# Kernel tuning notes

Hardware: AMD Instinct MI355X
Metric: run time of the kernel (lower is better)

The kernel has to match this reference:

```python
import jax, jax.numpy as jnp
import numpy as np

B, T, HID, H, Dk, Dv, K = 2, 1024, 1024, 8, 128, 128, 4
EPS = 1e-5


def _dwconv_causal(y, w, b):
    # y: [B,T,C], w: [C,1,K], b: [C]; torch Conv1d(padding=K-1) then [:, :, :T] == causal left-pad
    C = y.shape[-1]
    z = jnp.transpose(y, (0, 2, 1))  # [B,C,T]
    z = jax.lax.conv_general_dilated(
        z, w, window_strides=(1,), padding=[(K - 1, 0)],
        feature_group_count=C, dimension_numbers=("NCH", "OIH", "NCH"))
    z = z + b[None, :, None]
    return jnp.transpose(z, (0, 2, 1))


def _forward(x, Wq, Wk, Wv, conv_q_w, conv_q_b, conv_k_w, conv_k_b,
             conv_v_w, conv_v_b, Wa, ba, Wb, bb, Wg, Wo, ln_g, ln_b):
    b_, t_ = x.shape[0], x.shape[1]
    q = jax.nn.silu(_dwconv_causal(x @ Wq, conv_q_w, conv_q_b))
    k = jax.nn.silu(_dwconv_causal(x @ Wk, conv_k_w, conv_k_b))
    v = jax.nn.silu(_dwconv_causal(x @ Wv, conv_v_w, conv_v_b))
    q = q.reshape(b_, t_, H, Dk)
    k = k.reshape(b_, t_, H, Dk) * (Dk ** -0.5)
    v = v.reshape(b_, t_, H, Dv)
    alpha = jax.nn.sigmoid(x @ Wa + ba)  # [B,T,H]
    beta = jax.nn.sigmoid(x @ Wb + bb)   # [B,T,H]

    # time-major for scan
    qt = jnp.transpose(q, (1, 0, 2, 3))  # [T,B,H,Dk]
    kt = jnp.transpose(k, (1, 0, 2, 3))
    vt = jnp.transpose(v, (1, 0, 2, 3))  # [T,B,H,Dv]
    at = jnp.transpose(alpha, (1, 0, 2))  # [T,B,H]
    bt = jnp.transpose(beta, (1, 0, 2))

    def step(S, inp):
        q_t, k_t, v_t, a_t, b_t = inp
        sk = jnp.einsum('bhij,bhj->bhi', S, k_t)          # S @ k
        err = sk - v_t                                     # [B,H,Dv]
        S = a_t[:, :, None, None] * S - b_t[:, :, None, None] * (err[..., None] * k_t[:, :, None, :])
        o_t = jnp.einsum('bhij,bhj->bhi', S, q_t)          # S @ q (post-update)
        return S, o_t

    S0 = jnp.zeros((b_, H, Dv, Dk), x.dtype)
    _, o = jax.lax.scan(step, S0, (qt, kt, vt, at, bt))
    o = jnp.transpose(o, (1, 0, 2, 3))  # [B,T,H,Dv]

    # LayerNorm over Dv
    mu = jnp.mean(o, axis=-1, keepdims=True)
    var = jnp.mean((o - mu) ** 2, axis=-1, keepdims=True)
    o = (o - mu) * jax.lax.rsqrt(var + EPS) * ln_g + ln_b

    g = jax.nn.sigmoid(x @ Wg).reshape(b_, t_, H, Dv)
    o = (o * g).reshape(b_, t_, H * Dv)
    return o @ Wo


def setup_inputs() -> dict:
    key = jax.random.key(0)
    ks = jax.random.split(key, 18)
    s = 0.02

    def n(k, shape, scale=s):
        return jax.random.normal(k, shape, jnp.float32) * scale

    return {
        "x": jax.random.normal(ks[0], (B, T, HID), jnp.float32),
        "Wq": n(ks[1], (HID, H * Dk)),
        "Wk": n(ks[2], (HID, H * Dk)),
        "Wv": n(ks[3], (HID, H * Dv)),
        "conv_q_w": n(ks[4], (H * Dk, 1, K), 0.25),
        "conv_q_b": n(ks[5], (H * Dk,), 0.1),
        "conv_k_w": n(ks[6], (H * Dk, 1, K), 0.25),
        "conv_k_b": n(ks[7], (H * Dk,), 0.1),
        "conv_v_w": n(ks[8], (H * Dv, 1, K), 0.25),
        "conv_v_b": n(ks[9], (H * Dv,), 0.1),
        "Wa": n(ks[10], (HID, H)),
        "ba": n(ks[11], (H,), 0.1),
        "Wb": n(ks[12], (HID, H)),
        "bb": n(ks[13], (H,), 0.1),
        "Wg": n(ks[14], (HID, H * Dv)),
        "Wo": n(ks[15], (H * Dv, HID)),
        "ln_g": jnp.ones((Dv,), jnp.float32),
        "ln_b": jnp.zeros((Dv,), jnp.float32),
    }


def reference(x, Wq, Wk, Wv, conv_q_w, conv_q_b, conv_k_w, conv_k_b,
              conv_v_w, conv_v_b, Wa, ba, Wb, bb, Wg, Wo, ln_g, ln_b):
    return _forward(x, Wq, Wk, Wv, conv_q_w, conv_q_b, conv_k_w, conv_k_b,
                    conv_v_w, conv_v_b, Wa, ba, Wb, bb, Wg, Wo, ln_g, ln_b)
```

## Files before the change

### kernel.cpp

```cpp
#include <hip/hip_runtime.h>

#define TSEQ 1024
#define HID_ 1024
#define NH 8
#define DK 128
#define DV 128
#define ROWS 2048
#define SZf (ROWS * HID_)
#define LCH 64
#define NCK 16
#define KSTR 136
#define ESTR 65

typedef __attribute__((ext_vector_type(8))) short short8;
typedef __attribute__((ext_vector_type(4))) float f32x4;
#define MFMA __builtin_amdgcn_mfma_f32_16x16x32_bf16

__device__ __forceinline__ float sig_(float x) { return 1.f / (1.f + __expf(-x)); }

__device__ __forceinline__ ushort f2bf(float f) {
    unsigned int u = __builtin_bit_cast(unsigned int, f);
    u += 0x7FFF + ((u >> 16) & 1);
    return (ushort)(u >> 16);
}
__device__ __forceinline__ float bf2f(ushort u) {
    return __builtin_bit_cast(float, ((unsigned int)u) << 16);
}
__device__ __forceinline__ unsigned int pk2(float lo, float hi) {
    return (unsigned int)f2bf(lo) | ((unsigned int)f2bf(hi) << 16);
}

__device__ __forceinline__ void gload16(const void* g, void* l) {
    __builtin_amdgcn_global_load_lds(
        (const __attribute__((address_space(1))) unsigned int*)g,
        (__attribute__((address_space(3))) unsigned int*)l, 16, 0, 0);
}

__global__ __launch_bounds__(256)
void k_x2bf(const float* __restrict__ x, ushort* __restrict__ xb)
{
    const size_t i8 = (size_t)blockIdx.x * 256 + threadIdx.x;
    float4 v0 = *(const float4*)(x + i8 * 8);
    float4 v1 = *(const float4*)(x + i8 * 8 + 4);
    uint4 o;
    o.x = pk2(v0.x, v0.y); o.y = pk2(v0.z, v0.w);
    o.z = pk2(v1.x, v1.y); o.w = pk2(v1.z, v1.w);
    *(uint4*)(xb + i8 * 8) = o;
}

__global__ __launch_bounds__(256)
void k_wT(const float* __restrict__ s0, const float* __restrict__ s1,
          const float* __restrict__ s2, const float* __restrict__ s3,
          const float* __restrict__ s4,
          ushort* __restrict__ dst, ushort* __restrict__ dstWo)
{
    const int z = blockIdx.z;
    const float* W = (z == 0) ? s0 : (z == 1) ? s1 : (z == 2) ? s2
                   : (z == 3) ? s3 : s4;
    ushort* WT = (z < 4) ? dst + (size_t)z * (1024 * 1024) : dstWo;
    __shared__ float t[64][65];
    const int n0 = blockIdx.x * 64, k0 = blockIdx.y * 64;
    const int rr = threadIdx.x >> 4, cc = threadIdx.x & 15;
#pragma unroll
    for (int i = 0; i < 4; ++i) {
        const int row = i * 16 + rr;
        float4 v = *(const float4*)(W + (size_t)(k0 + row) * 1024 + n0 + cc * 4);
        t[row][cc * 4 + 0] = v.x; t[row][cc * 4 + 1] = v.y;
        t[row][cc * 4 + 2] = v.z; t[row][cc * 4 + 3] = v.w;
    }
    __syncthreads();
#pragma unroll
    for (int i = 0; i < 4; ++i) {
        const int n = i * 16 + rr;
        const int kc = cc * 4;
        ushort4 o;
        o.x = f2bf(t[kc + 0][n]); o.y = f2bf(t[kc + 1][n]);
        o.z = f2bf(t[kc + 2][n]); o.w = f2bf(t[kc + 3][n]);
        *(ushort4*)(WT + (size_t)(n0 + n) * 1024 + k0 + kc) = o;
    }
}

template<typename CT>
__device__ __forceinline__ void gemm_tile_mfma(const ushort* __restrict__ A,
                                               const ushort* __restrict__ BT,
                                               CT* __restrict__ C,
                                               int brow, int bcol)
{
    __shared__ ushort As[128 * 64];
    __shared__ ushort Bs[128 * 64];
    const int tid  = threadIdx.x;
    const int lane = tid & 63;
    const int wv   = tid >> 6;
    const int wm   = (wv >> 1) * 64;
    const int wn   = (wv & 1) * 64;
    const int l15  = lane & 15;
    const int lq   = lane >> 4;

    f32x4 acc[4][4];
#pragma unroll
    for (int i = 0; i < 4; ++i)
#pragma unroll
        for (int j = 0; j < 4; ++j)
#pragma unroll
            for (int e = 0; e < 4; ++e) acc[i][j][e] = 0.f;

    for (int k0 = 0; k0 < 1024; k0 += 64) {
        __syncthreads();
#pragma unroll
        for (int j = 0; j < 4; ++j) {
            const int idx  = j * 256 + tid;
            const int row  = idx >> 3;
            const int gcol = ((idx & 7) ^ (row & 7)) * 8;
            const int ldst = (j * 256 + wv * 64) * 8;
            gload16(A  + (size_t)(brow + row) * 1024 + k0 + gcol, As + ldst);
            gload16(BT + (size_t)(bcol + row) * 1024 + k0 + gcol, Bs + ldst);
        }
        __syncthreads();
#pragma unroll
        for (int kk = 0; kk < 2; ++kk) {
            short8 af[4], bf[4];
#pragma unroll
            for (int i = 0; i < 4; ++i) {
                const int ra = wm + i * 16 + l15;
                af[i] = *(const short8*)(As + ra * 64 + (((kk * 4 + lq) ^ (ra & 7)) * 8));
            }
#pragma unroll
            for (int j = 0; j < 4; ++j) {
                const int rb = wn + j * 16 + l15;
                bf[j] = *(const short8*)(Bs + rb * 64 + (((kk * 4 + lq) ^ (rb & 7)) * 8));
            }
#pragma unroll
            for (int i = 0; i < 4; ++i)
#pragma unroll
                for (int j = 0; j < 4; ++j)
                    acc[i][j] = MFMA(af[i], bf[j], acc[i][j], 0, 0, 0);
        }
    }
    const int l4 = lane >> 4;
#pragma unroll
    for (int i = 0; i < 4; ++i)
#pragma unroll
        for (int j = 0; j < 4; ++j)
#pragma unroll
            for (int r = 0; r < 4; ++r) {
                const size_t o = (size_t)(brow + wm + i * 16 + l4 * 4 + r) * 1024 +
                                 bcol + wn + j * 16 + l15;
                if constexpr (sizeof(CT) == 2) C[o] = f2bf(acc[i][j][r]);
                else                           C[o] = acc[i][j][r];
            }
}

__global__ __launch_bounds__(256)
void k_gemm4(const ushort* __restrict__ A, const ushort* __restrict__ WT,
             ushort* __restrict__ Cbase)
{
    const ushort* BT = WT + (size_t)blockIdx.z * (1024 * 1024);
    ushort* C = Cbase + (size_t)blockIdx.z * SZf;
    gemm_tile_mfma<ushort>(A, BT, C, blockIdx.y * 128, blockIdx.x * 128);
}

__global__ __launch_bounds__(256)
void k_gemm1(const ushort* __restrict__ A, const ushort* __restrict__ BT,
             float* __restrict__ C)
{
    gemm_tile_mfma<float>(A, BT, C, blockIdx.y * 128, blockIdx.x * 128);
}

__global__ __launch_bounds__(256)
void k_ab(const float* __restrict__ x, const float* __restrict__ Wa,
          const float* __restrict__ ba, const float* __restrict__ Wb,
          const float* __restrict__ bb, float* __restrict__ aT,
          float* __restrict__ bT)
{
    const int r = blockIdx.x * 4 + (threadIdx.x >> 6);
    const int lane = threadIdx.x & 63;
    const int b = r >> 10, t = r & 1023;
    const float* xr = x + (size_t)r * HID_;
    float acc[16];
#pragma unroll
    for (int n = 0; n < 16; ++n) acc[n] = 0.f;
    for (int c = lane; c < HID_; c += 64) {
        const float xv = xr[c];
        const float* wa = Wa + c * 8;
        const float* wb = Wb + c * 8;
#pragma unroll
        for (int n = 0; n < 8; ++n) {
            acc[n]     = fmaf(xv, wa[n], acc[n]);
            acc[8 + n] = fmaf(xv, wb[n], acc[8 + n]);
        }
    }
#pragma unroll
    for (int n = 0; n < 16; ++n) {
#pragma unroll
        for (int m = 32; m; m >>= 1) acc[n] += __shfl_xor(acc[n], m);
    }
    if (lane < 8) {
        aT[(size_t)(b * 8 + lane) * TSEQ + t] = sig_(acc[lane] + ba[lane]);
        bT[(size_t)(b * 8 + lane) * TSEQ + t] = sig_(acc[8 + lane] + bb[lane]);
    }
}

__global__ __launch_bounds__(256)
void k_convprep(const ushort* __restrict__ qb_, const ushort* __restrict__ kb_,
                const ushort* __restrict__ vb_,
                const float* __restrict__ wq, const float* __restrict__ bq,
                const float* __restrict__ wk, const float* __restrict__ bk,
                const float* __restrict__ wv, const float* __restrict__ bv,
                const float* __restrict__ aT, const float* __restrict__ bT,
                ushort* __restrict__ Kst, ushort* __restrict__ Qst,
                ushort* __restrict__ VstT, ushort* __restrict__ KTst,
                ushort* __restrict__ Mg, ushort* __restrict__ Gg,
                float* __restrict__ pug, float* __restrict__ pog,
                float* __restrict__ dtotg)
{
    const int cid = blockIdx.x;
    const int bh = cid >> 4, j = cid & 15;
    const int b = bh >> 3, h = bh & 7;
    const int tid = threadIdx.x;
    const int t0 = j * LCH;

    __shared__ ushort Kb[64 * KSTR], Qb[64 * KSTR];
    __shared__ ushort Vl[128 * 72];
    __shared__ float Ef[64 * ESTR];
    __shared__ float Mf[64 * ESTR];
    __shared__ float cums[64], bv2[64];

    if (tid >= 192) {
        const int lane = tid - 192;
        const float a = aT[(size_t)bh * TSEQ + t0 + lane];
        bv2[lane] = bT[(size_t)bh * TSEQ + t0 + lane];
        float cs = __logf(a);
#pragma unroll
        for (int d = 1; d < 64; d <<= 1) {
            float pv = __shfl_up(cs, d);
            if (lane >= d) cs += pv;
        }
        cums[lane] = cs;
    } else {
        const int z = tid >> 6;
        const int c2 = (tid & 63) * 2;
        const ushort* src  = (z == 0) ? qb_ : (z == 1) ? kb_ : vb_;
        const float* w     = (z == 0) ? wq : (z == 1) ? wk : wv;
        const float* bias  = (z == 0) ? bq : (z == 1) ? bk : bv;
        const float scale  = (z == 1) ? 0.08838834764831845f : 1.f;
        const int gc = h * 128 + c2;
        const float w0a = w[gc * 4],     w1a = w[gc * 4 + 1], w2a = w[gc * 4 + 2], w3a = w[gc * 4 + 3];
        const float w0b = w[gc * 4 + 4], w1b = w[gc * 4 + 5], w2b = w[gc * 4 + 6], w3b = w[gc * 4 + 7];
        const float bsa = bias[gc], bsb = bias[gc + 1];
        float ya0 = 0.f, ya1 = 0.f, ya2 = 0.f, yb0 = 0.f, yb1 = 0.f, yb2 = 0.f;
        if (j > 0) {
#pragma unroll
            for (int i = 0; i < 3; ++i) {
                uint u = *(const uint*)(src + (size_t)(b * TSEQ + t0 - 3 + i) * HID_ + gc);
                const float lo = bf2f((ushort)u), hi = bf2f((ushort)(u >> 16));
                if (i == 0) { ya0 = lo; yb0 = hi; }
                else if (i == 1) { ya1 = lo; yb1 = hi; }
                else { ya2 = lo; yb2 = hi; }
            }
        }
#pragma unroll 4
        for (int tl = 0; tl < 64; ++tl) {
            uint u = *(const uint*)(src + (size_t)(b * TSEQ + t0 + tl) * HID_ + gc);
            const float x0 = bf2f((ushort)u), x1 = bf2f((ushort)(u >> 16));
            float a0 = fmaf(w0a, ya0, fmaf(w1a, ya1, fmaf(w2a, ya2, fmaf(w3a, x0, bsa))));
            float a1 = fmaf(w0b, yb0, fmaf(w1b, yb1, fmaf(w2b, yb2, fmaf(w3b, x1, bsb))));
            const float s0 = a0 * sig_(a0) * scale;
            const float s1 = a1 * sig_(a1) * scale;
            if (z == 0)      *(uint*)(Qb + tl * KSTR + c2) = pk2(s0, s1);
            else if (z == 1) *(uint*)(Kb + tl * KSTR + c2) = pk2(s0, s1);
            else {
                Vl[(c2 + 0) * 72 + tl] = f2bf(s0);
                Vl[(c2 + 1) * 72 + tl] = f2bf(s1);
            }
            ya0 = ya1; ya1 = ya2; ya2 = x0;
            yb0 = yb1; yb1 = yb2; yb2 = x1;
        }
    }
    __syncthreads();

    const size_t go = (size_t)cid * 8192;
    const float ctop = cums[63];
#pragma unroll
    for (int jx = 0; jx < 4; ++jx) {
        const int i16 = tid + jx * 256;
        const int row = i16 >> 4, col = (i16 & 15) * 8;
        *(uint4*)(Kst + go + i16 * 8) = *(const uint4*)(Kb + row * KSTR + col);
        *(uint4*)(Qst + go + i16 * 8) = *(const uint4*)(Qb + row * KSTR + col);
    }
#pragma unroll
    for (int jx = 0; jx < 4; ++jx) {
        const int idx = tid + jx * 256;
        const int dv = idx >> 3, tq = (idx & 7) * 8;
        *(uint4*)(VstT + go + dv * 64 + tq) = *(const uint4*)(Vl + dv * 72 + tq);
        const int dk = idx >> 3, tt = (idx & 7) * 8;
        ushort tmp[8];
#pragma unroll
        for (int e = 0; e < 8; ++e)
            tmp[e] = f2bf(bf2f(Kb[(tt + e) * KSTR + dk]) * __expf(ctop - cums[tt + e]));
        *(uint4*)(KTst + go + dk * 64 + tt) = *(uint4*)tmp;
    }

    const int wv2 = tid >> 6, l = tid & 63, l15 = l & 15, lq = l >> 4;
    const int k8o = lq * 8;
    f32x4 accK[4], accQ4[4];
#pragma unroll
    for (int jx = 0; jx < 4; ++jx) {
        accK[jx] = f32x4{0.f, 0.f, 0.f, 0.f};
        accQ4[jx] = f32x4{0.f, 0.f, 0.f, 0.f};
    }
#pragma unroll
    for (int kk = 0; kk < 4; ++kk) {
        short8 aK = *(const short8*)(Kb + (wv2 * 16 + l15) * KSTR + kk * 32 + k8o);
        short8 aQ = *(const short8*)(Qb + (wv2 * 16 + l15) * KSTR + kk * 32 + k8o);
#pragma unroll
        for (int js = 0; js < 4; ++js) {
            short8 bK = *(const short8*)(Kb + (js * 16 + l15) * KSTR + kk * 32 + k8o);
            accK[js]  = MFMA(aK, bK, accK[js], 0, 0, 0);
            accQ4[js] = MFMA(aQ, bK, accQ4[js], 0, 0, 0);
        }
    }
    ushort* Gc = Gg + (size_t)cid * 4096;
#pragma unroll
    for (int js = 0; js < 4; ++js) {
#pragma unroll
        for (int r = 0; r < 4; ++r) {
            const int t = wv2 * 16 + lq * 4 + r;
            const int s = js * 16 + l15;
            const float cp = (t > 0) ? cums[t - 1] : 0.f;
            Ef[t * ESTR + s] = (s < t) ? __expf(cp - cums[s]) * accK[js][r] : 0.f;
            const float gv = (s <= t) ? __expf(cums[t] - cums[s]) * accQ4[js][r] : 0.f;
            Gc[t * 64 + s] = f2bf(gv);
        }
    }
    __syncthreads();

    if (tid < 64) {
        const int s = tid;
        for (int r = 0; r < 64; ++r) Mf[r * ESTR + s] = 0.f;
        Mf[s * ESTR + s] = bv2[s];
        for (int t = 1; t < 64; ++t) {
            float s0 = 0.f, s1 = 0.f;
            int r = 0;
            for (; r + 1 < t; r += 2) {
                s0 = fmaf(Ef[t * ESTR + r],     Mf[r * ESTR + s],       s0);
                s1 = fmaf(Ef[t * ESTR + r + 1], Mf[(r + 1) * ESTR + s], s1);
            }
            if (r < t) s0 = fmaf(Ef[t * ESTR + r], Mf[r * ESTR + s], s0);
            if (s < t) Mf[t * ESTR + s] = -bv2[t] * (s0 + s1);
        }
    }
    __syncthreads();
    ushort* Mc = Mg + (size_t)cid * 4096;
#pragma unroll
    for (int jx = 0; jx < 16; ++jx) {
        const int e = tid + jx * 256;
        Mc[e] = f2bf(Mf[(e >> 6) * ESTR + (e & 63)]);
    }
    if (tid < 64) {
        const float cp = (tid > 0) ? cums[tid - 1] : 0.f;
        pug[cid * 64 + tid] = __expf(cp);
        pog[cid * 64 + tid] = __expf(cums[tid]);
        if (tid == 0) dtotg[cid] = __expf(cums[63]);
    }
}

__global__ __launch_bounds__(256)
void k_scan2(const ushort* __restrict__ Kst, const ushort* __restrict__ KTst,
             const ushort* __restrict__ VstT, const ushort* __restrict__ Mg,
             const float* __restrict__ pug, const float* __restrict__ dtg,
             ushort* __restrict__ Sst, ushort* __restrict__ Wst)
{
    const int blk = blockIdx.x;
    const int bh = blk >> 1, half = blk & 1;
    const int tid = threadIdx.x;
    const int wv = tid >> 6, l = tid & 63, l15 = l & 15, lq = l >> 4;
    const int k8o = lq * 8;
    const int dvw = wv * 16;

    __shared__ ushort Kb[64 * KSTR];
    __shared__ ushort KTb[128 * 72];
    __shared__ ushort Mb[64 * 72];
    __shared__ ushort Vb[64 * 72];
    __shared__ ushort Shb[64 * KSTR], Slb[64 * KSTR];
    __shared__ ushort Yb[64 * 72], Wb[64 * 72];
    __shared__ float puv[64], dts[1];

    f32x4 accS[8];
#pragma unroll
    for (int m = 0; m < 8; ++m) accS[m] = f32x4{0.f, 0.f, 0.f, 0.f};

    uint4 rk[4], rkt[4], rm[2], rv[2];
    float rpu = 0.f, rdt = 0.f;

    auto LOADC = [&](int cc) {
        const int cid = bh * 16 + cc;
        const size_t go = (size_t)cid * 8192;
#pragma unroll
        for (int jx = 0; jx < 4; ++jx) {
            rk[jx]  = *(const uint4*)(Kst  + go + (tid + jx * 256) * 8);
            rkt[jx] = *(const uint4*)(KTst + go + (tid + jx * 256) * 8);
        }
#pragma unroll
        for (int jx = 0; jx < 2; ++jx) {
            rm[jx] = *(const uint4*)(Mg + (size_t)cid * 4096 + (tid + jx * 256) * 8);
            rv[jx] = *(const uint4*)(VstT + go + half * 4096 + (tid + jx * 256) * 8);
        }
        if (tid < 64) {
            rpu = pug[cid * 64 + tid];
            if (tid == 0) rdt = dtg[cid];
        }
    };
    auto WRITEC = [&]() {
#pragma unroll
        for (int jx = 0; jx < 4; ++jx) {
            const int i16 = tid + jx * 256;
            *(uint4*)(Kb  + (i16 >> 4) * KSTR + (i16 & 15) * 8) = rk[jx];
            *(uint4*)(KTb + (i16 >> 3) * 72   + (i16 & 7) * 8)  = rkt[jx];
        }
#pragma unroll
        for (int jx = 0; jx < 2; ++jx) {
            const int i8 = tid + jx * 256;
            *(uint4*)(Mb + (i8 >> 3) * 72 + (i8 & 7) * 8) = rm[jx];
            *(uint4*)(Vb + (i8 >> 3) * 72 + (i8 & 7) * 8) = rv[jx];
        }
        if (tid < 64) {
            puv[tid] = rpu;
            if (tid == 0) dts[0] = rdt;
        }
    };

    LOADC(0); WRITEC();
    __syncthreads();

    for (int c = 0; c < NCK; ++c) {
        if (c + 1 < NCK) LOADC(c + 1);

#pragma unroll
        for (int m = 0; m < 8; ++m) {
            ushort h4[4], l4v[4];
#pragma unroll
            for (int r = 0; r < 4; ++r) {
                const float sv = accS[m][r];
                const ushort hi = f2bf(sv);
                h4[r] = hi;
                l4v[r] = f2bf(sv - bf2f(hi));
            }
            *(uint2*)(Shb + (dvw + l15) * KSTR + m * 16 + lq * 4) = *(uint2*)h4;
            *(uint2*)(Slb + (dvw + l15) * KSTR + m * 16 + lq * 4) = *(uint2*)l4v;
        }
        f32x4 accU[4];
#pragma unroll
        for (int jj = 0; jj < 4; ++jj) accU[jj] = f32x4{0.f, 0.f, 0.f, 0.f};
#pragma unroll
        for (int kk = 0; kk < 4; ++kk) {
            short8 sh = *(const short8*)(Shb + (dvw + l15) * KSTR + kk * 32 + k8o);
            short8 sl = *(const short8*)(Slb + (dvw + l15) * KSTR + kk * 32 + k8o);
#pragma unroll
            for (int jj = 0; jj < 4; ++jj) {
                short8 ka = *(const short8*)(Kb + (jj * 16 + l15) * KSTR + kk * 32 + k8o);
                accU[jj] = MFMA(ka, sh, accU[jj], 0, 0, 0);
                accU[jj] = MFMA(ka, sl, accU[jj], 0, 0, 0);
            }
        }
#pragma unroll
        for (int jj = 0; jj < 4; ++jj) {
            float pu4[4];
            *(float4*)pu4 = *(const float4*)(puv + jj * 16 + lq * 4);
            ushort v4[4];
            *(uint2*)v4 = *(const uint2*)(Vb + (dvw + l15) * 72 + jj * 16 + lq * 4);
            ushort y4[4];
#pragma unroll
            for (int r = 0; r < 4; ++r)
                y4[r] = f2bf(bf2f(v4[r]) - pu4[r] * accU[jj][r]);
            *(uint2*)(Yb + (dvw + l15) * 72 + jj * 16 + lq * 4) = *(uint2*)y4;
        }
        f32x4 accW[4];
#pragma unroll
        for (int jj = 0; jj < 4; ++jj) accW[jj] = f32x4{0.f, 0.f, 0.f, 0.f};
#pragma unroll
        for (int kk = 0; kk < 2; ++kk) {
            short8 yb = *(const short8*)(Yb + (dvw + l15) * 72 + kk * 32 + k8o);
#pragma unroll
            for (int jj = 0; jj < 4; ++jj) {
                short8 mf = *(const short8*)(Mb + (jj * 16 + l15) * 72 + kk * 32 + k8o);
                accW[jj] = MFMA(mf, yb, accW[jj], 0, 0, 0);
            }
        }
#pragma unroll
        for (int jj = 0; jj < 4; ++jj) {
            ushort w4[4];
#pragma unroll
            for (int r = 0; r < 4; ++r)
                w4[r] = f2bf(accW[jj][r]);
            *(uint2*)(Wb + (dvw + l15) * 72 + jj * 16 + lq * 4) = *(uint2*)w4;
        }
        const float dt = dts[0];
#pragma unroll
        for (int m = 0; m < 8; ++m)
#pragma unroll
            for (int r = 0; r < 4; ++r) accS[m][r] *= dt;
#pragma unroll
        for (int kk = 0; kk < 2; ++kk) {
            short8 wc = *(const short8*)(Wb + (dvw + l15) * 72 + kk * 32 + k8o);
#pragma unroll
            for (int m = 0; m < 8; ++m) {
                short8 kt = *(const short8*)(KTb + (m * 16 + l15) * 72 + kk * 32 + k8o);
                accS[m] = MFMA(kt, wc, accS[m], 0, 0, 0);
            }
        }
        {
            const int cid = bh * 16 + c;
#pragma unroll
            for (int jx = 0; jx < 4; ++jx) {
                const int idx = l + jx * 64;
                const int dvo = idx >> 4, ko = (idx & 15) * 8;
                *(uint4*)(Sst + (size_t)cid * 16384 +
                          (half * 64 + dvw + dvo) * 128 + ko) =
                    *(const uint4*)(Shb + (dvw + dvo) * KSTR + ko);
            }
#pragma unroll
            for (int jx = 0; jx < 2; ++jx) {
                const int idx = l + jx * 64;
                const int dvo = idx >> 3, t8 = (idx & 7) * 8;
                *(uint4*)(Wst + (size_t)cid * 8192 +
                          (half * 64 + dvw + dvo) * 64 + t8) =
                    *(const uint4*)(Wb + (dvw + dvo) * 72 + t8);
            }
        }
        __syncthreads();
        if (c + 1 < NCK) WRITEC();
        __syncthreads();
    }
}

__global__ __launch_bounds__(256)
void k_out(const ushort* __restrict__ Sst, const ushort* __restrict__ Qst,
           const ushort* __restrict__ Gg, const ushort* __restrict__ Wst,
           const float* __restrict__ pog, const ushort* __restrict__ gb_,
           const float* __restrict__ lng, const float* __restrict__ lnb,
           ushort* __restrict__ ogb)
{
    const int cid = blockIdx.x;
    const int bh = cid >> 4, c = cid & 15;
    const int b = bh >> 3, h = bh & 7;
    const int t0 = c * LCH;
    const int tid = threadIdx.x;
    const int wv = tid >> 6, l = tid & 63, l15 = l & 15, lq = l >> 4;
    const int k8o = lq * 8;

    __shared__ ushort Sb[128 * KSTR];
    __shared__ ushort Qb[64 * KSTR];
    __shared__ ushort Gb[64 * 72];
    __shared__ ushort Wqb[128 * 72];
    __shared__ float  Ot[64 * 132];
    __shared__ float  pov[64];

#pragma unroll
    for (int jx = 0; jx < 8; ++jx) {
        const int i16 = tid + jx * 256;
        *(uint4*)(Sb + (i16 >> 4) * KSTR + (i16 & 15) * 8) =
            *(const uint4*)(Sst + (size_t)cid * 16384 + i16 * 8);
    }
#pragma unroll
    for (int jx = 0; jx < 4; ++jx) {
        const int i16 = tid + jx * 256;
        *(uint4*)(Qb + (i16 >> 4) * KSTR + (i16 & 15) * 8) =
            *(const uint4*)(Qst + (size_t)cid * 8192 + i16 * 8);
        *(uint4*)(Wqb + (i16 >> 3) * 72 + (i16 & 7) * 8) =
            *(const uint4*)(Wst + (size_t)cid * 8192 + i16 * 8);
    }
#pragma unroll
    for (int jx = 0; jx < 2; ++jx) {
        const int i8 = tid + jx * 256;
        *(uint4*)(Gb + (i8 >> 3) * 72 + (i8 & 7) * 8) =
            *(const uint4*)(Gg + (size_t)cid * 4096 + i8 * 8);
    }
    if (tid < 64) pov[tid] = pog[cid * 64 + tid];
    __syncthreads();

#pragma unroll
    for (int i = 0; i < 2; ++i) {
        const int dvt = wv * 2 + i;
        f32x4 acc[4], acg[4];
#pragma unroll
        for (int jj = 0; jj < 4; ++jj) {
            acc[jj] = f32x4{0.f, 0.f, 0.f, 0.f};
            acg[jj] = f32x4{0.f, 0.f, 0.f, 0.f};
        }
#pragma unroll
        for (int kk = 0; kk < 4; ++kk) {
            short8 sa = *(const short8*)(Sb + (dvt * 16 + l15) * KSTR + kk * 32 + k8o);
#pragma unroll
            for (int jj = 0; jj < 4; ++jj) {
                short8 qb = *(const short8*)(Qb + (jj * 16 + l15) * KSTR + kk * 32 + k8o);
                acc[jj] = MFMA(sa, qb, acc[jj], 0, 0, 0);
            }
        }
#pragma unroll
        for (int kk = 0; kk < 2; ++kk) {
            short8 wa = *(const short8*)(Wqb + (dvt * 16 + l15) * 72 + kk * 32 + k8o);
#pragma unroll
            for (int jj = 0; jj < 4; ++jj) {
                short8 gb = *(const short8*)(Gb + (jj * 16 + l15) * 72 + kk * 32 + k8o);
                acg[jj] = MFMA(wa, gb, acg[jj], 0, 0, 0);
            }
        }
#pragma unroll
        for (int jj = 0; jj < 4; ++jj) {
            const int t = jj * 16 + l15;
            const float po = pov[t];
            float4 o4;
            o4.x = po * acc[jj][0] + acg[jj][0];
            o4.y = po * acc[jj][1] + acg[jj][1];
            o4.z = po * acc[jj][2] + acg[jj][2];
            o4.w = po * acc[jj][3] + acg[jj][3];
            *(float4*)(Ot + t * 132 + dvt * 16 + lq * 4) = o4;
        }
    }
    __syncthreads();

    const int d = l * 2;
    const float lg0 = lng[d], lg1 = lng[d + 1];
    const float lb0 = lnb[d], lb1 = lnb[d + 1];
    const size_t btbase = (size_t)b * TSEQ + t0 + wv * 16;
#pragma unroll 1
    for (int rr = 0; rr < 16; ++rr) {
        const int t = wv * 16 + rr;
        float2 xv = *(const float2*)(Ot + t * 132 + d);
        float s = xv.x + xv.y;
#pragma unroll
        for (int m = 32; m; m >>= 1) s += __shfl_xor(s, m);
        const float mu = s * (1.f / 128.f);
        const float d0 = xv.x - mu, d1 = xv.y - mu;
        float v = d0 * d0 + d1 * d1;
#pragma unroll
        for (int m = 32; m; m >>= 1) v += __shfl_xor(v, m);
        const float inv = rsqrtf(v * (1.f / 128.f) + 1e-5f);
        const uint gu = *(const uint*)(gb_ + (btbase + rr) * HID_ + h * DV + d);
        const float g0 = sig_(bf2f((ushort)gu)), g1 = sig_(bf2f((ushort)(gu >> 16)));
        const float y0 = (d0 * inv * lg0 + lb0) * g0;
        const float y1 = (d1 * inv * lg1 + lb1) * g1;
        *(uint*)(ogb + (btbase + rr) * HID_ + h * DV + d) = pk2(y0, y1);
    }
}

extern "C" void kernel_launch(void* const* d_in, const int* in_sizes, int n_in,
                              void* d_out, int out_size, void* d_ws, size_t ws_size,
                              hipStream_t stream)
{
    const float* x   = (const float*)d_in[0];
    const float* Wq  = (const float*)d_in[1];
    const float* Wk  = (const float*)d_in[2];
    const float* Wv  = (const float*)d_in[3];
    const float* cqw = (const float*)d_in[4];
    const float* cqb = (const float*)d_in[5];
    const float* ckw = (const float*)d_in[6];
    const float* ckb = (const float*)d_in[7];
    const float* cvw = (const float*)d_in[8];
    const float* cvb = (const float*)d_in[9];
    const float* Wa  = (const float*)d_in[10];
    const float* ba  = (const float*)d_in[11];
    const float* Wb  = (const float*)d_in[12];
    const float* bb  = (const float*)d_in[13];
    const float* Wg  = (const float*)d_in[14];
    const float* Wo  = (const float*)d_in[15];
    const float* lng = (const float*)d_in[16];
    const float* lnb = (const float*)d_in[17];
    float* out = (float*)d_out;
    float* ws  = (float*)d_ws;

    ushort* qb_ = (ushort*)ws;
    ushort* kb_ = qb_ + (size_t)SZf;
    ushort* vb_ = qb_ + (size_t)2 * SZf;
    ushort* gb_ = qb_ + (size_t)3 * SZf;

    ushort* ogb  = (ushort*)(ws + 2 * (size_t)SZf);
    ushort* VstT = ogb + (size_t)2 * 1024 * 1024;
    ushort* WoT  = (ushort*)(ws + 3 * (size_t)SZf);
    float*  o_buf = ws + 4 * (size_t)SZf;
    ushort* WT4  = (ushort*)o_buf;
    ushort* Sst  = (ushort*)o_buf;
    float* aT  = ws + 5 * (size_t)SZf;
    float* bT  = aT + 16 * TSEQ;
    float* pug = bT + 16 * TSEQ;
    float* pog = pug + 256 * 64;
    float* dtg = pog + 256 * 64;

    float*  tail = ws + 5 * (size_t)SZf + 131072;
    ushort* Kst  = (ushort*)tail;
    ushort* Qst  = Kst + (size_t)256 * 8192;
    ushort* xbf  = Qst + (size_t)256 * 8192;
    ushort* KTst = xbf;

    ushort* Mg  = (ushort*)out;
    ushort* Gg  = Mg + (size_t)256 * 4096;
    ushort* Wst = Gg + (size_t)256 * 4096;

    k_x2bf<<<1024, 256, 0, stream>>>(x, xbf);
    k_wT<<<dim3(16, 16, 5), 256, 0, stream>>>(Wq, Wk, Wv, Wg, Wo, WT4, WoT);
    k_gemm4<<<dim3(8, 16, 4), 256, 0, stream>>>(xbf, WT4, qb_);
    k_ab<<<512, 256, 0, stream>>>(x, Wa, ba, Wb, bb, aT, bT);
    k_convprep<<<256, 256, 0, stream>>>(qb_, kb_, vb_,
                                        cqw, cqb, ckw, ckb, cvw, cvb,
                                        aT, bT, Kst, Qst, VstT, KTst,
                                        Mg, Gg, pug, pog, dtg);
    k_scan2<<<32, 256, 0, stream>>>(Kst, KTst, VstT, Mg, pug, dtg, Sst, Wst);
    k_out<<<256, 256, 0, stream>>>(Sst, Qst, Gg, Wst, pog, gb_, lng, lnb, ogb);
    k_gemm1<<<dim3(8, 16), 256, 0, stream>>>(ogb, WoT, out);
}
```

Measured before the change: 211.1 us.

## Keep M-solve in registers and overlap chunk stores with the triangular solve

The per-chunk triangular M recurrence now keeps each column in a 64-float register array and reads E rows as float4 (ESTR padded to 68 for alignment), so the shared Mf buffer and one barrier go away. While wave 0 runs this serial solve, the other three waves write the K/Q/V/KT chunk tiles to global memory, which previously happened before the MFMA stage on all waves. The decay scale factors and the pug/pog/dtot outputs are computed during the prefix scan via shuffles. This raises register pressure on wave 0 and unbalances work across waves.

```diff
diff --git a/kernel.cpp b/kernel.cpp
--- a/kernel.cpp
+++ b/kernel.cpp
@@ -10,7 +10,7 @@
 #define LCH 64
 #define NCK 16
 #define KSTR 136
-#define ESTR 65
+#define ESTR 68
 
 typedef __attribute__((ext_vector_type(8))) short short8;
 typedef __attribute__((ext_vector_type(4))) float f32x4;
@@ -222,8 +222,7 @@
     __shared__ ushort Kb[64 * KSTR], Qb[64 * KSTR];
     __shared__ ushort Vl[128 * 72];
     __shared__ float Ef[64 * ESTR];
-    __shared__ float Mf[64 * ESTR];
-    __shared__ float cums[64], bv2[64];
+    __shared__ float cums[64], bv2[64], cv_s[64];
 
     if (tid >= 192) {
         const int lane = tid - 192;
@@ -236,6 +235,12 @@
             if (lane >= d) cs += pv;
         }
         cums[lane] = cs;
+        const float cp = __shfl_up(cs, 1);
+        const float ctop = __shfl(cs, 63);
+        pug[cid * 64 + lane] = (lane > 0) ? __expf(cp) : 1.f;
+        pog[cid * 64 + lane] = __expf(cs);
+        cv_s[lane] = __expf(ctop - cs);
+        if (lane == 0) dtotg[cid] = __expf(ctop);
     } else {
         const int z = tid >> 6;
         const int c2 = (tid & 63) * 2;
@@ -278,28 +283,6 @@
     }
     __syncthreads();
 
-    const size_t go = (size_t)cid * 8192;
-    const float ctop = cums[63];
-#pragma unroll
-    for (int jx = 0; jx < 4; ++jx) {
-        const int i16 = tid + jx * 256;
-        const int row = i16 >> 4, col = (i16 & 15) * 8;
-        *(uint4*)(Kst + go + i16 * 8) = *(const uint4*)(Kb + row * KSTR + col);
-        *(uint4*)(Qst + go + i16 * 8) = *(const uint4*)(Qb + row * KSTR + col);
-    }
-#pragma unroll
-    for (int jx = 0; jx < 4; ++jx) {
-        const int idx = tid + jx * 256;
-        const int dv = idx >> 3, tq = (idx & 7) * 8;
-        *(uint4*)(VstT + go + dv * 64 + tq) = *(const uint4*)(Vl + dv * 72 + tq);
-        const int dk = idx >> 3, tt = (idx & 7) * 8;
-        ushort tmp[8];
-#pragma unroll
-        for (int e = 0; e < 8; ++e)
-            tmp[e] = f2bf(bf2f(Kb[(tt + e) * KSTR + dk]) * __expf(ctop - cums[tt + e]));
-        *(uint4*)(KTst + go + dk * 64 + tt) = *(uint4*)tmp;
-    }
-
     const int wv2 = tid >> 6, l = tid & 63, l15 = l & 15, lq = l >> 4;
     const int k8o = lq * 8;
     f32x4 accK[4], accQ4[4];
@@ -334,33 +317,50 @@
     }
     __syncthreads();
 
-    if (tid < 64) {
-        const int s = tid;
-        for (int r = 0; r < 64; ++r) Mf[r * ESTR + s] = 0.f;
-        Mf[s * ESTR + s] = bv2[s];
+    const size_t go = (size_t)cid * 8192;
+    if (wv2 == 0) {
+        const int s = l;
+        ushort* Mc = Mg + (size_t)cid * 4096;
+        float Mreg[64];
+        const float bvs = bv2[s];
+#pragma unroll
+        for (int r = 0; r < 64; ++r) Mreg[r] = (r == s) ? bvs : 0.f;
+#pragma unroll
         for (int t = 1; t < 64; ++t) {
-            float s0 = 0.f, s1 = 0.f;
-            int r = 0;
-            for (; r + 1 < t; r += 2) {
-                s0 = fmaf(Ef[t * ESTR + r],     Mf[r * ESTR + s],       s0);
-                s1 = fmaf(Ef[t * ESTR + r + 1], Mf[(r + 1) * ESTR + s], s1);
-            }
-            if (r < t) s0 = fmaf(Ef[t * ESTR + r], Mf[r * ESTR + s], s0);
-            if (s < t) Mf[t * ESTR + s] = -bv2[t] * (s0 + s1);
-        }
-    }
-    __syncthreads();
-    ushort* Mc = Mg + (size_t)cid * 4096;
-#pragma unroll
-    for (int jx = 0; jx < 16; ++jx) {
-        const int e = tid + jx * 256;
-        Mc[e] = f2bf(Mf[(e >> 6) * ESTR + (e & 63)]);
-    }
-    if (tid < 64) {
-        const float cp = (tid > 0) ? cums[tid - 1] : 0.f;
-        pug[cid * 64 + tid] = __expf(cp);
-        pog[cid * 64 + tid] = __expf(cums[tid]);
-        if (tid == 0) dtotg[cid] = __expf(cums[63]);
+            float a0 = 0.f, a1 = 0.f, a2 = 0.f, a3 = 0.f;
+#pragma unroll
+            for (int r4 = 0; r4 < 64; r4 += 4) {
+                if (r4 < t) {
+                    float4 e = *(const float4*)(Ef + t * ESTR + r4);
+                    if (r4 + 0 < t) a0 = fmaf(e.x, Mreg[r4 + 0], a0);
+                    if (r4 + 1 < t) a1 = fmaf(e.y, Mreg[r4 + 1], a1);
+                    if (r4 + 2 < t) a2 = fmaf(e.z, Mreg[r4 + 2], a2);
+                    if (r4 + 3 < t) a3 = fmaf(e.w, Mreg[r4 + 3], a3);
+                }
+            }
+            const float mt = -bv2[t] * ((a0 + a1) + (a2 + a3));
+            Mreg[t] = (s < t) ? mt : Mreg[t];
+        }
+#pragma unroll
+        for (int r = 0; r < 64; ++r)
+            Mc[r * 64 + s] = f2bf(Mreg[r]);
+    } else {
+        const int st = tid - 64;
+        for (int i = st; i < 1024; i += 192) {
+            const int row = i >> 4, col = (i & 15) * 8;
+            *(uint4*)(Kst + go + i * 8) = *(const uint4*)(Kb + row * KSTR + col);
+            *(uint4*)(Qst + go + i * 8) = *(const uint4*)(Qb + row * KSTR + col);
+        }
+        for (int i = st; i < 1024; i += 192) {
+            const int dv = i >> 3, tq = (i & 7) * 8;
+            *(uint4*)(VstT + go + dv * 64 + tq) = *(const uint4*)(Vl + dv * 72 + tq);
+            const int dk = i >> 3, tt = (i & 7) * 8;
+            ushort tmp[8];
+#pragma unroll
+            for (int e = 0; e < 8; ++e)
+                tmp[e] = f2bf(bf2f(Kb[(tt + e) * KSTR + dk]) * cv_s[tt + e]);
+            *(uint4*)(KTst + go + dk * 64 + tt) = *(uint4*)tmp;
+        }
     }
 }
 
```

After: 232.8 us. 10.3% more time.
